# Kernel optimization log

Measured on AMD Instinct MI355X. Metric: run time of the kernel, lower is better.

Reference implementation:

```python
import jax, jax.numpy as jnp
import numpy as np

EPS = 1e-5

def gamma_layer_norm(x, gamma):
    # LayerNorm over last dim with learnable gamma only (no bias)
    mu = jnp.mean(x, axis=-1, keepdims=True)
    var = jnp.var(x, axis=-1, keepdims=True)
    return (x - mu) * jax.lax.rsqrt(var + EPS) * gamma

def setup_inputs() -> dict:
    key = jax.random.key(0)
    k1, k2, k3, k4 = jax.random.split(key, 4)
    b, n, dim = 8, 4096, 512
    heads, head_size = 8, 64
    hidden = heads * head_size  # 512
    x = jax.random.normal(k1, (b, n, dim), dtype=jnp.float32)
    # nn.Linear(dim, hidden*3, bias=False): weight [3*hidden, dim]
    w_qkv = jax.random.normal(k2, (3 * hidden, dim), dtype=jnp.float32) * (dim ** -0.5)
    # nn.Linear(hidden, dim, bias=False): weight [dim, hidden]
    w_out = jax.random.normal(k3, (dim, hidden), dtype=jnp.float32) * (hidden ** -0.5)
    gamma = 1.0 + 0.02 * jax.random.normal(k4, (dim,), dtype=jnp.float32)
    return {"x": x, "w_qkv": w_qkv, "w_out": w_out, "gamma": gamma}

def reference(x, w_qkv, w_out, gamma):
    b, n, dim = x.shape
    heads, head_size = 8, 64
    scale = head_size ** -0.5
    # norm=False -> Identity; no time conditioning
    qkv = jnp.einsum('bnd,hd->bnh', x, w_qkv)  # [b, n, 3*hidden]
    q, k, v = jnp.split(qkv, 3, axis=-1)
    def to_heads(t):
        return t.reshape(b, n, heads, head_size).transpose(0, 2, 1, 3)  # b h n d
    q, k, v = to_heads(q), to_heads(k), to_heads(v)
    q = jax.nn.softmax(q, axis=-1) * scale   # softmax over feature dim
    k = jax.nn.softmax(k, axis=-2)           # softmax over sequence dim
    context = jnp.einsum('bhnd,bhne->bhde', k, v)      # [b, h, d, e]
    out = jnp.einsum('bhde,bhnd->bhne', context, q)    # [b, h, n, e]
    out = out.transpose(0, 2, 1, 3).reshape(b, n, heads * head_size)
    out = jnp.einsum('bnh,dh->bnd', out, w_out)
    out = gamma_layer_norm(out, gamma)  # dropout inactive (p=0 / eval)
    return out
```

## Files before the change

kernel.cpp:

```cpp
#include <hip/hip_runtime.h>
#include <hip/hip_bf16.h>
#include <stdint.h>
#include <stddef.h>

typedef __bf16 bf16_t;
typedef __bf16 bf16x8 __attribute__((ext_vector_type(8)));
typedef __bf16 bf16x4 __attribute__((ext_vector_type(4)));
typedef float floatx4 __attribute__((ext_vector_type(4)));

#define DIM 512
#define SEQ 4096
#define BATCH 8
#define BK 32
#define LDP 40

static __device__ __forceinline__ floatx4 mfma_bf16(bf16x8 a, bf16x8 b, floatx4 c) {
  return __builtin_amdgcn_mfma_f32_16x16x32_bf16(a, b, c, 0, 0, 0);
}

typedef __attribute__((address_space(1))) const void* gas_ptr;
typedef __attribute__((address_space(3))) void* las_ptr;
static __device__ __forceinline__ void gll16(const void* g, void* l) {
  __builtin_amdgcn_global_load_lds((gas_ptr)g, (las_ptr)l, 16, 0, 0);
}

__global__ __launch_bounds__(256) void k_cvt_w(const float* __restrict__ w, bf16_t* __restrict__ wb) {
  int i = (blockIdx.x * 256 + threadIdx.x) * 8;
  float4 a = *(const float4*)&w[i];
  float4 b = *(const float4*)&w[i + 4];
  bf16x8 o;
  o[0] = (bf16_t)a.x; o[1] = (bf16_t)a.y; o[2] = (bf16_t)a.z; o[3] = (bf16_t)a.w;
  o[4] = (bf16_t)b.x; o[5] = (bf16_t)b.y; o[6] = (bf16_t)b.z; o[7] = (bf16_t)b.w;
  *(bf16x8*)&wb[i] = o;
}

__global__ __launch_bounds__(256) void k_qkv(const float* __restrict__ X,
                                             const bf16_t* __restrict__ Wb,
                                             bf16_t* __restrict__ qs,
                                             bf16_t* __restrict__ ek,
                                             bf16_t* __restrict__ vb,
                                             float* __restrict__ S) {
  __shared__ __align__(16) float  Asf[128 * BK];
  __shared__ __align__(16) bf16_t Bs [128 * BK];
  const int tid = threadIdx.x;
  const int lane = tid & 63;
  const int w = tid >> 6;
  const int wr = w >> 1, wc = w & 1;
  const int l15 = lane & 15, l4 = lane >> 4;
  const int m0 = blockIdx.x * 128;
  const int n0 = blockIdx.y * 128;

  const float* gA = X + (size_t)(m0 + w * 32 + (lane >> 3)) * DIM
                      + (((lane & 7) ^ (lane >> 3)) << 2);
  const bf16_t* gB = Wb + (size_t)(n0 + w * 32 + (lane >> 2)) * DIM
                        + ((((lane & 3) ^ ((lane >> 2) & 3))) << 3);
  float*  lA = &Asf[(w * 32) * BK];
  bf16_t* lB = &Bs [(w * 32) * BK];

  floatx4 acc[4][4];
#pragma unroll
  for (int i = 0; i < 4; ++i)
#pragma unroll
    for (int j = 0; j < 4; ++j) acc[i][j] = (floatx4){0.f, 0.f, 0.f, 0.f};

  for (int kt = 0; kt < DIM; kt += BK) {
    gll16(gA,            lA);
    gll16(gA + 8 * DIM,  lA + 8 * BK);
    gll16(gA + 16 * DIM, lA + 16 * BK);
    gll16(gA + 24 * DIM, lA + 24 * BK);
    gll16(gB,            lB);
    gll16(gB + 16 * DIM, lB + 16 * BK);
    gA += BK; gB += BK;
    __syncthreads();
    bf16x8 af[4], bfr[4];
#pragma unroll
    for (int f = 0; f < 4; ++f) {
      int ar = wr * 64 + f * 16 + l15;
      int u0 = (l4 * 2) ^ (ar & 7);
      int u1 = (l4 * 2 + 1) ^ (ar & 7);
      float4 a0 = *(const float4*)&Asf[ar * BK + u0 * 4];
      float4 a1 = *(const float4*)&Asf[ar * BK + u1 * 4];
      bf16x8 t;
      t[0] = (bf16_t)a0.x; t[1] = (bf16_t)a0.y; t[2] = (bf16_t)a0.z; t[3] = (bf16_t)a0.w;
      t[4] = (bf16_t)a1.x; t[5] = (bf16_t)a1.y; t[6] = (bf16_t)a1.z; t[7] = (bf16_t)a1.w;
      af[f] = t;
      int br = wc * 64 + f * 16 + l15;
      int bu = l4 ^ (br & 3);
      bfr[f] = *(const bf16x8*)&Bs[br * BK + bu * 8];
    }
#pragma unroll
    for (int i = 0; i < 4; ++i)
#pragma unroll
      for (int j = 0; j < 4; ++j)
        acc[i][j] = mfma_bf16(af[i], bfr[j], acc[i][j]);
    __syncthreads();
  }

  const int colbase = n0 + wc * 64;
  if (n0 < 512) {
#pragma unroll
    for (int fm = 0; fm < 4; ++fm) {
#pragma unroll
      for (int r = 0; r < 4; ++r) {
        float v0 = acc[fm][0][r], v1 = acc[fm][1][r], v2 = acc[fm][2][r], v3 = acc[fm][3][r];
        float mx = fmaxf(fmaxf(v0, v1), fmaxf(v2, v3));
        mx = fmaxf(mx, __shfl_xor(mx, 1));
        mx = fmaxf(mx, __shfl_xor(mx, 2));
        mx = fmaxf(mx, __shfl_xor(mx, 4));
        mx = fmaxf(mx, __shfl_xor(mx, 8));
        float e0 = __expf(v0 - mx), e1 = __expf(v1 - mx), e2 = __expf(v2 - mx), e3 = __expf(v3 - mx);
        float s = e0 + e1 + e2 + e3;
        s += __shfl_xor(s, 1); s += __shfl_xor(s, 2); s += __shfl_xor(s, 4); s += __shfl_xor(s, 8);
        float inv = 0.125f / s;
        int m = m0 + wr * 64 + fm * 16 + l4 * 4 + r;
        bf16_t* rowp = qs + (size_t)m * DIM + colbase;
        rowp[l15]      = (bf16_t)(e0 * inv);
        rowp[16 + l15] = (bf16_t)(e1 * inv);
        rowp[32 + l15] = (bf16_t)(e2 * inv);
        rowp[48 + l15] = (bf16_t)(e3 * inv);
      }
    }
  } else if (n0 < 1024) {
    const int cb = colbase - 512;
    float c0 = 0.f, c1 = 0.f, c2 = 0.f, c3 = 0.f;
#pragma unroll
    for (int fm = 0; fm < 4; ++fm) {
#pragma unroll
      for (int r = 0; r < 4; ++r) {
        int m = m0 + wr * 64 + fm * 16 + l4 * 4 + r;
        bf16_t* rowp = ek + (size_t)m * DIM + cb;
        float e0 = __expf(acc[fm][0][r]);
        float e1 = __expf(acc[fm][1][r]);
        float e2 = __expf(acc[fm][2][r]);
        float e3 = __expf(acc[fm][3][r]);
        rowp[l15]      = (bf16_t)e0;
        rowp[16 + l15] = (bf16_t)e1;
        rowp[32 + l15] = (bf16_t)e2;
        rowp[48 + l15] = (bf16_t)e3;
        c0 += e0; c1 += e1; c2 += e2; c3 += e3;
      }
    }
    c0 += __shfl_xor(c0, 16); c0 += __shfl_xor(c0, 32);
    c1 += __shfl_xor(c1, 16); c1 += __shfl_xor(c1, 32);
    c2 += __shfl_xor(c2, 16); c2 += __shfl_xor(c2, 32);
    c3 += __shfl_xor(c3, 16); c3 += __shfl_xor(c3, 32);
    if (lane < 16) {
      int b = m0 >> 12;
      atomicAdd(&S[b * 512 + cb + lane],      c0);
      atomicAdd(&S[b * 512 + cb + 16 + lane], c1);
      atomicAdd(&S[b * 512 + cb + 32 + lane], c2);
      atomicAdd(&S[b * 512 + cb + 48 + lane], c3);
    }
  } else {
    const int cb = colbase - 1024;
#pragma unroll
    for (int fm = 0; fm < 4; ++fm) {
#pragma unroll
      for (int r = 0; r < 4; ++r) {
        int m = m0 + wr * 64 + fm * 16 + l4 * 4 + r;
        bf16_t* rowp = vb + (size_t)m * DIM + cb;
        rowp[l15]      = (bf16_t)acc[fm][0][r];
        rowp[16 + l15] = (bf16_t)acc[fm][1][r];
        rowp[32 + l15] = (bf16_t)acc[fm][2][r];
        rowp[48 + l15] = (bf16_t)acc[fm][3][r];
      }
    }
  }
}

#define TP 136
__global__ __launch_bounds__(256) void k_ctx(const bf16_t* __restrict__ ek,
                                             const bf16_t* __restrict__ vb,
                                             float* __restrict__ ctxpart) {
  __shared__ __align__(16) bf16_t ekT[64 * TP];
  __shared__ __align__(16) bf16_t vT[64 * TP];
  __shared__ float red[4096];
  const int tid = threadIdx.x;
  const int lane = tid & 63, wid = tid >> 6;
  const int l15 = lane & 15, l4 = lane >> 4;
  const int bh = blockIdx.x, chunk = blockIdx.y;
  const int b = bh >> 3, h = bh & 7;
  const int base = b * SEQ + chunk * 512;

  floatx4 acc[4][4];
#pragma unroll
  for (int i = 0; i < 4; ++i)
#pragma unroll
    for (int j = 0; j < 4; ++j) acc[i][j] = (floatx4){0.f, 0.f, 0.f, 0.f};

  for (int nt = 0; nt < 4; ++nt) {
    const int n0 = base + nt * 128;
#pragma unroll
    for (int i = 0; i < 4; ++i) {
      int q = tid + i * 256;
      int n = q & 127;
      int c8 = (q >> 7) << 3;
      bf16x8 vk = *(const bf16x8*)&ek[(size_t)(n0 + n) * DIM + h * 64 + c8];
      bf16x8 vv = *(const bf16x8*)&vb[(size_t)(n0 + n) * DIM + h * 64 + c8];
#pragma unroll
      for (int j = 0; j < 8; ++j) {
        ekT[(c8 + j) * TP + n] = vk[j];
        vT [(c8 + j) * TP + n] = vv[j];
      }
    }
    __syncthreads();
    const int nb = wid * 32;
    bf16x8 af[4], bfr[4];
#pragma unroll
    for (int f = 0; f < 4; ++f) {
      af[f]  = *(const bf16x8*)&ekT[(f * 16 + l15) * TP + nb + l4 * 8];
      bfr[f] = *(const bf16x8*)&vT [(f * 16 + l15) * TP + nb + l4 * 8];
    }
#pragma unroll
    for (int i = 0; i < 4; ++i)
#pragma unroll
      for (int j = 0; j < 4; ++j)
        acc[i][j] = mfma_bf16(af[i], bfr[j], acc[i][j]);
    __syncthreads();
  }

  for (int w = 0; w < 4; ++w) {
    if (wid == w) {
#pragma unroll
      for (int fm = 0; fm < 4; ++fm)
#pragma unroll
        for (int fn = 0; fn < 4; ++fn)
#pragma unroll
          for (int r = 0; r < 4; ++r) {
            int d = fm * 16 + l4 * 4 + r;
            int e = fn * 16 + l15;
            if (w == 0) red[d * 64 + e] = acc[fm][fn][r];
            else        red[d * 64 + e] += acc[fm][fn][r];
          }
    }
    __syncthreads();
  }
  float* dst = ctxpart + ((size_t)bh * 8 + chunk) * 4096;
#pragma unroll
  for (int i = 0; i < 4; ++i) {
    int q = tid + i * 256;
    *(float4*)&dst[q * 4] = *(const float4*)&red[q * 4];
  }
}

__global__ __launch_bounds__(256) void k_ctxred(const float* __restrict__ ctxpart,
                                                const float* __restrict__ S,
                                                float* __restrict__ ctx) {
  int bh = blockIdx.x;
  int idx = blockIdx.y * 256 + threadIdx.x;
  int b = bh >> 3, h = bh & 7;
  float s = 0.f;
#pragma unroll
  for (int p = 0; p < 8; ++p) s += ctxpart[((size_t)bh * 8 + p) * 4096 + idx];
  int d = idx >> 6;
  ctx[(size_t)bh * 4096 + idx] = s / S[b * 512 + h * 64 + d];
}

__global__ __launch_bounds__(128) void k_mt(const float* __restrict__ ctx,
                                            const float* __restrict__ w_out,
                                            bf16_t* __restrict__ Mt) {
  __shared__ float cs[4096];
  const int tid = threadIdx.x;
  const int b = blockIdx.x, h = blockIdx.y, dq = blockIdx.z;
#pragma unroll
  for (int i = 0; i < 8; ++i) {
    int q = tid + i * 128;
    *(float4*)&cs[q * 4] = *(const float4*)&ctx[((size_t)(b * 8 + h)) * 4096 + q * 4];
  }
  __syncthreads();
  const int dcol = dq * 128 + tid;
  float a[64];
#pragma unroll
  for (int d = 0; d < 64; ++d) a[d] = 0.f;
  for (int e = 0; e < 64; ++e) {
    float we = w_out[(size_t)dcol * 512 + h * 64 + e];
#pragma unroll
    for (int d = 0; d < 64; ++d) a[d] += cs[d * 64 + e] * we;
  }
  bf16_t* dst = Mt + ((size_t)b * 512 + dcol) * 512 + h * 64;
#pragma unroll
  for (int g = 0; g < 8; ++g) {
    bf16x8 o;
#pragma unroll
    for (int j = 0; j < 8; ++j) o[j] = (bf16_t)a[g * 8 + j];
    *(bf16x8*)&dst[g * 8] = o;
  }
}

__global__ __launch_bounds__(256) void k_out(const bf16_t* __restrict__ qs,
                                             const bf16_t* __restrict__ Mt,
                                             float* __restrict__ out2) {
  __shared__ __align__(16) bf16_t As2[128 * BK];
  __shared__ __align__(16) bf16_t Bs2[128 * BK];
  const int tid = threadIdx.x;
  const int lane = tid & 63, w = tid >> 6;
  const int wr = w >> 1, wc = w & 1;
  const int l15 = lane & 15, l4 = lane >> 4;
  const int m0 = blockIdx.x * 128;
  const int n0 = blockIdx.y * 128;
  const bf16_t* Bp = Mt + (size_t)(blockIdx.x >> 5) * 512 * 512;

  const int srow = lane >> 2;
  const int sunit = (lane & 3) ^ (srow & 3);
  const bf16_t* gA = qs + (size_t)(m0 + w * 32 + srow) * 512 + (sunit << 3);
  const bf16_t* gB = Bp + (size_t)(n0 + w * 32 + srow) * 512 + (sunit << 3);
  bf16_t* lA = &As2[(w * 32) * BK];
  bf16_t* lB = &Bs2[(w * 32) * BK];

  floatx4 acc[4][4];
#pragma unroll
  for (int i = 0; i < 4; ++i)
#pragma unroll
    for (int j = 0; j < 4; ++j) acc[i][j] = (floatx4){0.f, 0.f, 0.f, 0.f};

  for (int kt = 0; kt < 512; kt += BK) {
    gll16(gA,            lA);
    gll16(gA + 16 * 512, lA + 16 * BK);
    gll16(gB,            lB);
    gll16(gB + 16 * 512, lB + 16 * BK);
    gA += BK; gB += BK;
    __syncthreads();
    bf16x8 af[4], bfr[4];
#pragma unroll
    for (int f = 0; f < 4; ++f) {
      int ar = wr * 64 + f * 16 + l15;
      int au = l4 ^ (ar & 3);
      af[f] = *(const bf16x8*)&As2[ar * BK + au * 8];
      int br = wc * 64 + f * 16 + l15;
      int bu = l4 ^ (br & 3);
      bfr[f] = *(const bf16x8*)&Bs2[br * BK + bu * 8];
    }
#pragma unroll
    for (int i = 0; i < 4; ++i)
#pragma unroll
      for (int j = 0; j < 4; ++j)
        acc[i][j] = mfma_bf16(af[i], bfr[j], acc[i][j]);
    __syncthreads();
  }
#pragma unroll
  for (int fm = 0; fm < 4; ++fm) {
#pragma unroll
    for (int r = 0; r < 4; ++r) {
      int m = m0 + wr * 64 + fm * 16 + l4 * 4 + r;
      float* rowp = out2 + (size_t)m * 512 + n0 + wc * 64;
      rowp[l15]      = acc[fm][0][r];
      rowp[16 + l15] = acc[fm][1][r];
      rowp[32 + l15] = acc[fm][2][r];
      rowp[48 + l15] = acc[fm][3][r];
    }
  }
}

__global__ __launch_bounds__(256) void k_ln(const float* __restrict__ out2,
                                            const float* __restrict__ gamma,
                                            float* __restrict__ out) {
  const int lane = threadIdx.x & 63;
  const int row = blockIdx.x * 4 + (threadIdx.x >> 6);
  const float* x = out2 + (size_t)row * 512;
  float4 v0 = ((const float4*)x)[lane];
  float4 v1 = ((const float4*)x)[lane + 64];
  float s = v0.x + v0.y + v0.z + v0.w + v1.x + v1.y + v1.z + v1.w;
  float q = v0.x * v0.x + v0.y * v0.y + v0.z * v0.z + v0.w * v0.w
          + v1.x * v1.x + v1.y * v1.y + v1.z * v1.z + v1.w * v1.w;
#pragma unroll
  for (int m = 1; m <= 32; m <<= 1) { s += __shfl_xor(s, m); q += __shfl_xor(q, m); }
  float mean = s * (1.f / 512.f);
  float var = q * (1.f / 512.f) - mean * mean;
  float rstd = rsqrtf(var + 1e-5f);
  float4 g0 = ((const float4*)gamma)[lane];
  float4 g1 = ((const float4*)gamma)[lane + 64];
  float4 o0, o1;
  o0.x = (v0.x - mean) * rstd * g0.x;
  o0.y = (v0.y - mean) * rstd * g0.y;
  o0.z = (v0.z - mean) * rstd * g0.z;
  o0.w = (v0.w - mean) * rstd * g0.w;
  o1.x = (v1.x - mean) * rstd * g1.x;
  o1.y = (v1.y - mean) * rstd * g1.y;
  o1.z = (v1.z - mean) * rstd * g1.z;
  o1.w = (v1.w - mean) * rstd * g1.w;
  float* y = out + (size_t)row * 512;
  ((float4*)y)[lane] = o0;
  ((float4*)y)[lane + 64] = o1;
}

extern "C" void kernel_launch(void* const* d_in, const int* in_sizes, int n_in,
                              void* d_out, int out_size, void* d_ws, size_t ws_size,
                              hipStream_t stream) {
  const float* x     = (const float*)d_in[0];
  const float* w_qkv = (const float*)d_in[1];
  const float* w_out = (const float*)d_in[2];
  const float* gamma = (const float*)d_in[3];
  float* out = (float*)d_out;
  char* ws = (char*)d_ws;

  bf16_t* qs      = (bf16_t*)(ws);
  bf16_t* ek      = (bf16_t*)(ws + 33554432);
  bf16_t* vb      = (bf16_t*)(ws + 67108864);
  bf16_t* wqkvb   = (bf16_t*)(ws + 100663296);
  float*  S       = (float*)(ws + 102236160);
  float*  ctx     = (float*)(ws + 102252544);
  float*  ctxpart = (float*)(ws + 103301120);
  bf16_t* Mt      = (bf16_t*)(ws + 111689728);
  float*  out2    = (float*)(ws + 33554432);

  hipMemsetAsync(S, 0, BATCH * 512 * sizeof(float), stream);

  k_cvt_w<<<384, 256, 0, stream>>>(w_qkv, wqkvb);

  dim3 g1(256, 12);
  k_qkv<<<g1, 256, 0, stream>>>(x, wqkvb, qs, ek, vb, S);

  dim3 g2(64, 8);
  k_ctx<<<g2, 256, 0, stream>>>(ek, vb, ctxpart);

  dim3 g3(64, 16);
  k_ctxred<<<g3, 256, 0, stream>>>(ctxpart, S, ctx);

  dim3 g4(8, 8, 4);
  k_mt<<<g4, 128, 0, stream>>>(ctx, w_out, Mt);

  dim3 g5(256, 4);
  k_out<<<g5, 256, 0, stream>>>(qs, Mt, out2);

  k_ln<<<8192, 256, 0, stream>>>(out2, gamma, out);
}
```

Measured before the change: 203.6 us.

## Deepen GEMM K-tile to 64, store output projection as bf16, optionally pre-convert X

Both GEMM kernels now load 64-wide K slices per barrier with an 8-way XOR swizzle, which halves the number of sync/load rounds. The qkv kernel can optionally read a bf16 copy of X made by a separate conversion pass, used only when the workspace is large enough. The output projection result is written as bf16, halving intermediate traffic into the layernorm kernel at some precision cost. The larger tiles raise LDS use per block and may lower occupancy.

```diff
diff --git a/kernel.cpp b/kernel.cpp
--- a/kernel.cpp
+++ b/kernel.cpp
@@ -5,14 +5,11 @@
 
 typedef __bf16 bf16_t;
 typedef __bf16 bf16x8 __attribute__((ext_vector_type(8)));
-typedef __bf16 bf16x4 __attribute__((ext_vector_type(4)));
 typedef float floatx4 __attribute__((ext_vector_type(4)));
 
 #define DIM 512
 #define SEQ 4096
 #define BATCH 8
-#define BK 32
-#define LDP 40
 
 static __device__ __forceinline__ floatx4 mfma_bf16(bf16x8 a, bf16x8 b, floatx4 c) {
   return __builtin_amdgcn_mfma_f32_16x16x32_bf16(a, b, c, 0, 0, 0);
@@ -24,7 +21,7 @@
   __builtin_amdgcn_global_load_lds((gas_ptr)g, (las_ptr)l, 16, 0, 0);
 }
 
-__global__ __launch_bounds__(256) void k_cvt_w(const float* __restrict__ w, bf16_t* __restrict__ wb) {
+__global__ __launch_bounds__(256) void k_cvt(const float* __restrict__ w, bf16_t* __restrict__ wb) {
   int i = (blockIdx.x * 256 + threadIdx.x) * 8;
   float4 a = *(const float4*)&w[i];
   float4 b = *(const float4*)&w[i + 4];
@@ -34,14 +31,16 @@
   *(bf16x8*)&wb[i] = o;
 }
 
+template<bool XB>
 __global__ __launch_bounds__(256) void k_qkv(const float* __restrict__ X,
+                                             const bf16_t* __restrict__ Xb,
                                              const bf16_t* __restrict__ Wb,
                                              bf16_t* __restrict__ qs,
                                              bf16_t* __restrict__ ek,
                                              bf16_t* __restrict__ vb,
                                              float* __restrict__ S) {
-  __shared__ __align__(16) float  Asf[128 * BK];
-  __shared__ __align__(16) bf16_t Bs [128 * BK];
+  __shared__ __align__(16) char Abuf[XB ? (128 * 64 * 2) : (128 * 64 * 4)];
+  __shared__ __align__(16) bf16_t Bs[128 * 64];
   const int tid = threadIdx.x;
   const int lane = tid & 63;
   const int w = tid >> 6;
@@ -50,12 +49,15 @@
   const int m0 = blockIdx.x * 128;
   const int n0 = blockIdx.y * 128;
 
-  const float* gA = X + (size_t)(m0 + w * 32 + (lane >> 3)) * DIM
-                      + (((lane & 7) ^ (lane >> 3)) << 2);
-  const bf16_t* gB = Wb + (size_t)(n0 + w * 32 + (lane >> 2)) * DIM
-                        + ((((lane & 3) ^ ((lane >> 2) & 3))) << 3);
-  float*  lA = &Asf[(w * 32) * BK];
-  bf16_t* lB = &Bs [(w * 32) * BK];
+  const bf16_t* gB = Wb + (size_t)(n0 + w * 32 + (lane >> 3)) * DIM + (((lane & 7) ^ (lane >> 3)) << 3);
+  bf16_t* lB = Bs + (w * 32) * 64 + lane * 8;
+
+  const bf16_t* gAb = Xb + (size_t)(m0 + w * 32 + (lane >> 3)) * DIM + (((lane & 7) ^ (lane >> 3)) << 3);
+  bf16_t* lAb = (bf16_t*)Abuf + (w * 32) * 64 + lane * 8;
+  const int r4 = lane >> 4, uu = lane & 15;
+  const float* gA0 = X + (size_t)(m0 + w * 32 + r4) * DIM + ((uu ^ r4) << 2);
+  const float* gA1 = X + (size_t)(m0 + w * 32 + r4) * DIM + ((uu ^ (4 | r4)) << 2);
+  float* lAf = (float*)Abuf + (w * 32) * 64 + lane * 4;
 
   floatx4 acc[4][4];
 #pragma unroll
@@ -63,36 +65,52 @@
 #pragma unroll
     for (int j = 0; j < 4; ++j) acc[i][j] = (floatx4){0.f, 0.f, 0.f, 0.f};
 
-  for (int kt = 0; kt < DIM; kt += BK) {
-    gll16(gA,            lA);
-    gll16(gA + 8 * DIM,  lA + 8 * BK);
-    gll16(gA + 16 * DIM, lA + 16 * BK);
-    gll16(gA + 24 * DIM, lA + 24 * BK);
-    gll16(gB,            lB);
-    gll16(gB + 16 * DIM, lB + 16 * BK);
-    gA += BK; gB += BK;
-    __syncthreads();
-    bf16x8 af[4], bfr[4];
-#pragma unroll
-    for (int f = 0; f < 4; ++f) {
-      int ar = wr * 64 + f * 16 + l15;
-      int u0 = (l4 * 2) ^ (ar & 7);
-      int u1 = (l4 * 2 + 1) ^ (ar & 7);
-      float4 a0 = *(const float4*)&Asf[ar * BK + u0 * 4];
-      float4 a1 = *(const float4*)&Asf[ar * BK + u1 * 4];
-      bf16x8 t;
-      t[0] = (bf16_t)a0.x; t[1] = (bf16_t)a0.y; t[2] = (bf16_t)a0.z; t[3] = (bf16_t)a0.w;
-      t[4] = (bf16_t)a1.x; t[5] = (bf16_t)a1.y; t[6] = (bf16_t)a1.z; t[7] = (bf16_t)a1.w;
-      af[f] = t;
-      int br = wc * 64 + f * 16 + l15;
-      int bu = l4 ^ (br & 3);
-      bfr[f] = *(const bf16x8*)&Bs[br * BK + bu * 8];
-    }
-#pragma unroll
-    for (int i = 0; i < 4; ++i)
-#pragma unroll
-      for (int j = 0; j < 4; ++j)
-        acc[i][j] = mfma_bf16(af[i], bfr[j], acc[i][j]);
+  for (int kt = 0; kt < DIM; kt += 64) {
+    if constexpr (XB) {
+#pragma unroll
+      for (int i = 0; i < 4; ++i) gll16(gAb + i * 8 * DIM, lAb + i * 8 * 64);
+      gAb += 64;
+    } else {
+#pragma unroll
+      for (int i = 0; i < 8; ++i) {
+        const float* s = ((i & 1) ? gA1 : gA0) + i * 4 * DIM;
+        gll16(s, lAf + i * 4 * 64);
+      }
+      gA0 += 64; gA1 += 64;
+    }
+#pragma unroll
+    for (int i = 0; i < 4; ++i) gll16(gB + i * 8 * DIM, lB + i * 8 * 64);
+    gB += 64;
+    __syncthreads();
+#pragma unroll
+    for (int kk = 0; kk < 2; ++kk) {
+      bf16x8 af[4], bfr[4];
+#pragma unroll
+      for (int f = 0; f < 4; ++f) {
+        int ar = wr * 64 + f * 16 + l15;
+        if constexpr (XB) {
+          int ua = (kk * 4 + l4) ^ (l15 & 7);
+          af[f] = *(const bf16x8*)((const bf16_t*)Abuf + ar * 64 + ua * 8);
+        } else {
+          int u0 = (kk * 8 + l4 * 2) ^ (l15 & 7);
+          int u1 = (kk * 8 + l4 * 2 + 1) ^ (l15 & 7);
+          float4 a0 = *(const float4*)((const float*)Abuf + ar * 64 + u0 * 4);
+          float4 a1 = *(const float4*)((const float*)Abuf + ar * 64 + u1 * 4);
+          bf16x8 t;
+          t[0] = (bf16_t)a0.x; t[1] = (bf16_t)a0.y; t[2] = (bf16_t)a0.z; t[3] = (bf16_t)a0.w;
+          t[4] = (bf16_t)a1.x; t[5] = (bf16_t)a1.y; t[6] = (bf16_t)a1.z; t[7] = (bf16_t)a1.w;
+          af[f] = t;
+        }
+        int br = wc * 64 + f * 16 + l15;
+        int ub = (kk * 4 + l4) ^ (l15 & 7);
+        bfr[f] = *(const bf16x8*)(Bs + br * 64 + ub * 8);
+      }
+#pragma unroll
+      for (int i = 0; i < 4; ++i)
+#pragma unroll
+        for (int j = 0; j < 4; ++j)
+          acc[i][j] = mfma_bf16(af[i], bfr[j], acc[i][j]);
+    }
     __syncthreads();
   }
 
@@ -289,9 +307,9 @@
 
 __global__ __launch_bounds__(256) void k_out(const bf16_t* __restrict__ qs,
                                              const bf16_t* __restrict__ Mt,
-                                             float* __restrict__ out2) {
-  __shared__ __align__(16) bf16_t As2[128 * BK];
-  __shared__ __align__(16) bf16_t Bs2[128 * BK];
+                                             bf16_t* __restrict__ out2b) {
+  __shared__ __align__(16) bf16_t As[128 * 64];
+  __shared__ __align__(16) bf16_t Bs[128 * 64];
   const int tid = threadIdx.x;
   const int lane = tid & 63, w = tid >> 6;
   const int wr = w >> 1, wc = w & 1;
@@ -300,12 +318,10 @@
   const int n0 = blockIdx.y * 128;
   const bf16_t* Bp = Mt + (size_t)(blockIdx.x >> 5) * 512 * 512;
 
-  const int srow = lane >> 2;
-  const int sunit = (lane & 3) ^ (srow & 3);
-  const bf16_t* gA = qs + (size_t)(m0 + w * 32 + srow) * 512 + (sunit << 3);
-  const bf16_t* gB = Bp + (size_t)(n0 + w * 32 + srow) * 512 + (sunit << 3);
-  bf16_t* lA = &As2[(w * 32) * BK];
-  bf16_t* lB = &Bs2[(w * 32) * BK];
+  const bf16_t* gA = qs + (size_t)(m0 + w * 32 + (lane >> 3)) * 512 + (((lane & 7) ^ (lane >> 3)) << 3);
+  const bf16_t* gB = Bp + (size_t)(n0 + w * 32 + (lane >> 3)) * 512 + (((lane & 7) ^ (lane >> 3)) << 3);
+  bf16_t* lA = As + (w * 32) * 64 + lane * 8;
+  bf16_t* lB = Bs + (w * 32) * 64 + lane * 8;
 
   floatx4 acc[4][4];
 #pragma unroll
@@ -313,28 +329,32 @@
 #pragma unroll
     for (int j = 0; j < 4; ++j) acc[i][j] = (floatx4){0.f, 0.f, 0.f, 0.f};
 
-  for (int kt = 0; kt < 512; kt += BK) {
-    gll16(gA,            lA);
-    gll16(gA + 16 * 512, lA + 16 * BK);
-    gll16(gB,            lB);
-    gll16(gB + 16 * 512, lB + 16 * BK);
-    gA += BK; gB += BK;
-    __syncthreads();
-    bf16x8 af[4], bfr[4];
-#pragma unroll
-    for (int f = 0; f < 4; ++f) {
-      int ar = wr * 64 + f * 16 + l15;
-      int au = l4 ^ (ar & 3);
-      af[f] = *(const bf16x8*)&As2[ar * BK + au * 8];
-      int br = wc * 64 + f * 16 + l15;
-      int bu = l4 ^ (br & 3);
-      bfr[f] = *(const bf16x8*)&Bs2[br * BK + bu * 8];
-    }
-#pragma unroll
-    for (int i = 0; i < 4; ++i)
-#pragma unroll
-      for (int j = 0; j < 4; ++j)
-        acc[i][j] = mfma_bf16(af[i], bfr[j], acc[i][j]);
+  for (int kt = 0; kt < 512; kt += 64) {
+#pragma unroll
+    for (int i = 0; i < 4; ++i) {
+      gll16(gA + i * 8 * 512, lA + i * 8 * 64);
+      gll16(gB + i * 8 * 512, lB + i * 8 * 64);
+    }
+    gA += 64; gB += 64;
+    __syncthreads();
+#pragma unroll
+    for (int kk = 0; kk < 2; ++kk) {
+      bf16x8 af[4], bfr[4];
+#pragma unroll
+      for (int f = 0; f < 4; ++f) {
+        int ar = wr * 64 + f * 16 + l15;
+        int ua = (kk * 4 + l4) ^ (l15 & 7);
+        af[f] = *(const bf16x8*)(As + ar * 64 + ua * 8);
+        int br = wc * 64 + f * 16 + l15;
+        int ub = (kk * 4 + l4) ^ (l15 & 7);
+        bfr[f] = *(const bf16x8*)(Bs + br * 64 + ub * 8);
+      }
+#pragma unroll
+      for (int i = 0; i < 4; ++i)
+#pragma unroll
+        for (int j = 0; j < 4; ++j)
+          acc[i][j] = mfma_bf16(af[i], bfr[j], acc[i][j]);
+    }
     __syncthreads();
   }
 #pragma unroll
@@ -342,45 +362,46 @@
 #pragma unroll
     for (int r = 0; r < 4; ++r) {
       int m = m0 + wr * 64 + fm * 16 + l4 * 4 + r;
-      float* rowp = out2 + (size_t)m * 512 + n0 + wc * 64;
-      rowp[l15]      = acc[fm][0][r];
-      rowp[16 + l15] = acc[fm][1][r];
-      rowp[32 + l15] = acc[fm][2][r];
-      rowp[48 + l15] = acc[fm][3][r];
-    }
-  }
-}
-
-__global__ __launch_bounds__(256) void k_ln(const float* __restrict__ out2,
+      bf16_t* rowp = out2b + (size_t)m * 512 + n0 + wc * 64;
+      rowp[l15]      = (bf16_t)acc[fm][0][r];
+      rowp[16 + l15] = (bf16_t)acc[fm][1][r];
+      rowp[32 + l15] = (bf16_t)acc[fm][2][r];
+      rowp[48 + l15] = (bf16_t)acc[fm][3][r];
+    }
+  }
+}
+
+__global__ __launch_bounds__(256) void k_ln(const bf16_t* __restrict__ out2b,
                                             const float* __restrict__ gamma,
                                             float* __restrict__ out) {
   const int lane = threadIdx.x & 63;
   const int row = blockIdx.x * 4 + (threadIdx.x >> 6);
-  const float* x = out2 + (size_t)row * 512;
-  float4 v0 = ((const float4*)x)[lane];
-  float4 v1 = ((const float4*)x)[lane + 64];
-  float s = v0.x + v0.y + v0.z + v0.w + v1.x + v1.y + v1.z + v1.w;
-  float q = v0.x * v0.x + v0.y * v0.y + v0.z * v0.z + v0.w * v0.w
-          + v1.x * v1.x + v1.y * v1.y + v1.z * v1.z + v1.w * v1.w;
+  bf16x8 v = *(const bf16x8*)(out2b + (size_t)row * 512 + lane * 8);
+  float f[8];
+#pragma unroll
+  for (int j = 0; j < 8; ++j) f[j] = (float)v[j];
+  float s = 0.f, q = 0.f;
+#pragma unroll
+  for (int j = 0; j < 8; ++j) { s += f[j]; q += f[j] * f[j]; }
 #pragma unroll
   for (int m = 1; m <= 32; m <<= 1) { s += __shfl_xor(s, m); q += __shfl_xor(q, m); }
   float mean = s * (1.f / 512.f);
   float var = q * (1.f / 512.f) - mean * mean;
   float rstd = rsqrtf(var + 1e-5f);
-  float4 g0 = ((const float4*)gamma)[lane];
-  float4 g1 = ((const float4*)gamma)[lane + 64];
+  float4 g0 = ((const float4*)gamma)[lane * 2];
+  float4 g1 = ((const float4*)gamma)[lane * 2 + 1];
   float4 o0, o1;
-  o0.x = (v0.x - mean) * rstd * g0.x;
-  o0.y = (v0.y - mean) * rstd * g0.y;
-  o0.z = (v0.z - mean) * rstd * g0.z;
-  o0.w = (v0.w - mean) * rstd * g0.w;
-  o1.x = (v1.x - mean) * rstd * g1.x;
-  o1.y = (v1.y - mean) * rstd * g1.y;
-  o1.z = (v1.z - mean) * rstd * g1.z;
-  o1.w = (v1.w - mean) * rstd * g1.w;
+  o0.x = (f[0] - mean) * rstd * g0.x;
+  o0.y = (f[1] - mean) * rstd * g0.y;
+  o0.z = (f[2] - mean) * rstd * g0.z;
+  o0.w = (f[3] - mean) * rstd * g0.w;
+  o1.x = (f[4] - mean) * rstd * g1.x;
+  o1.y = (f[5] - mean) * rstd * g1.y;
+  o1.z = (f[6] - mean) * rstd * g1.z;
+  o1.w = (f[7] - mean) * rstd * g1.w;
   float* y = out + (size_t)row * 512;
-  ((float4*)y)[lane] = o0;
-  ((float4*)y)[lane + 64] = o1;
+  ((float4*)y)[lane * 2]     = o0;
+  ((float4*)y)[lane * 2 + 1] = o1;
 }
 
 extern "C" void kernel_launch(void* const* d_in, const int* in_sizes, int n_in,
@@ -398,17 +419,25 @@
   bf16_t* vb      = (bf16_t*)(ws + 67108864);
   bf16_t* wqkvb   = (bf16_t*)(ws + 100663296);
   float*  S       = (float*)(ws + 102236160);
+  bf16_t* Xb      = (bf16_t*)(ws + 102252544);
   float*  ctx     = (float*)(ws + 102252544);
   float*  ctxpart = (float*)(ws + 103301120);
   bf16_t* Mt      = (bf16_t*)(ws + 111689728);
-  float*  out2    = (float*)(ws + 33554432);
+  bf16_t* out2b   = (bf16_t*)(ws + 33554432);
+
+  const bool big = ws_size >= (size_t)135806976;
 
   hipMemsetAsync(S, 0, BATCH * 512 * sizeof(float), stream);
 
-  k_cvt_w<<<384, 256, 0, stream>>>(w_qkv, wqkvb);
+  k_cvt<<<384, 256, 0, stream>>>(w_qkv, wqkvb);
 
   dim3 g1(256, 12);
-  k_qkv<<<g1, 256, 0, stream>>>(x, wqkvb, qs, ek, vb, S);
+  if (big) {
+    k_cvt<<<8192, 256, 0, stream>>>(x, Xb);
+    k_qkv<true><<<g1, 256, 0, stream>>>(x, Xb, wqkvb, qs, ek, vb, S);
+  } else {
+    k_qkv<false><<<g1, 256, 0, stream>>>(x, (const bf16_t*)nullptr, wqkvb, qs, ek, vb, S);
+  }
 
   dim3 g2(64, 8);
   k_ctx<<<g2, 256, 0, stream>>>(ek, vb, ctxpart);
@@ -420,7 +449,7 @@
   k_mt<<<g4, 128, 0, stream>>>(ctx, w_out, Mt);
 
   dim3 g5(256, 4);
-  k_out<<<g5, 256, 0, stream>>>(qs, Mt, out2);
-
-  k_ln<<<8192, 256, 0, stream>>>(out2, gamma, out);
-}
+  k_out<<<g5, 256, 0, stream>>>(qs, Mt, out2b);
+
+  k_ln<<<8192, 256, 0, stream>>>(out2b, gamma, out);
+}
```

Result: faster. 198.8 us (-2.3%).
